# Performance work log

Measured on AMD Instinct MI355X. Metric: run time of the kernel, lower is better.

## Reference

```python
import jax, jax.numpy as jnp
import numpy as np

H = 768
NH = 12
HD = 64
FF = 3072
EPS = 1e-12


def layer_norm(x, g, b):
    mu = jnp.mean(x, axis=-1, keepdims=True)
    var = jnp.mean((x - mu) ** 2, axis=-1, keepdims=True)
    return (x - mu) * jax.lax.rsqrt(var + EPS) * g + b


def setup_inputs() -> dict:
    key = jax.random.key(0)
    ks = jax.random.split(key, 16)
    B, S, L = 16, 512, 50
    s = 0.02
    return {
        "hidden_states": jax.random.normal(ks[0], (B, S, H), jnp.float32),
        "attention_mask": jnp.zeros((B, 1, 1, S), jnp.float32),
        "past_key": jax.random.normal(ks[1], (B, NH, L, HD), jnp.float32),
        "past_value": jax.random.normal(ks[2], (B, NH, L, HD), jnp.float32),
        "Wq": jax.random.normal(ks[3], (H, H), jnp.float32) * s,
        "bq": jnp.zeros((H,), jnp.float32),
        "Wk": jax.random.normal(ks[4], (H, H), jnp.float32) * s,
        "bk": jnp.zeros((H,), jnp.float32),
        "Wv": jax.random.normal(ks[5], (H, H), jnp.float32) * s,
        "bv": jnp.zeros((H,), jnp.float32),
        "Wo": jax.random.normal(ks[6], (H, H), jnp.float32) * s,
        "bo": jnp.zeros((H,), jnp.float32),
        "ln1_g": jnp.ones((H,), jnp.float32),
        "ln1_b": jnp.zeros((H,), jnp.float32),
        "Wi": jax.random.normal(ks[7], (H, FF), jnp.float32) * s,
        "bi": jnp.zeros((FF,), jnp.float32),
        "Wf": jax.random.normal(ks[8], (FF, H), jnp.float32) * s,
        "bf": jnp.zeros((H,), jnp.float32),
        "ln2_g": jnp.ones((H,), jnp.float32),
        "ln2_b": jnp.zeros((H,), jnp.float32),
    }


def reference(hidden_states, attention_mask, past_key, past_value,
              Wq, bq, Wk, bk, Wv, bv, Wo, bo, ln1_g, ln1_b,
              Wi, bi, Wf, bf, ln2_g, ln2_b):
    B, S, _ = hidden_states.shape
    L = past_key.shape[2]

    def heads(x):  # [B,S,H] -> [B,NH,S,HD]
        return x.reshape(B, S, NH, HD).transpose(0, 2, 1, 3)

    q = heads(hidden_states @ Wq + bq)
    k = heads(hidden_states @ Wk + bk)
    v = heads(hidden_states @ Wv + bv)

    # faithful to source bug: past_key_values[0] concatenated into BOTH k and v
    k = jnp.concatenate([past_key, k], axis=2)  # [B,NH,L+S,HD]
    v = jnp.concatenate([past_key, v], axis=2)

    scores = jnp.einsum('bhqd,bhkd->bhqk', q, k) / jnp.sqrt(jnp.float32(HD))
    # visual mask positions get +1.0 (torch.ones), faithful to source
    vis_mask = jnp.ones((B, 1, 1, L), scores.dtype)
    full_mask = jnp.concatenate([vis_mask, attention_mask], axis=-1)
    scores = scores + full_mask

    probs = jax.nn.softmax(scores, axis=-1)
    ctx = jnp.einsum('bhqk,bhkd->bhqd', probs, v)  # [B,NH,S,HD]
    ctx = ctx.transpose(0, 2, 1, 3).reshape(B, S, H)

    attn_out = layer_norm(ctx @ Wo + bo + hidden_states, ln1_g, ln1_b)

    inter = jax.nn.gelu(attn_out @ Wi + bi, approximate=False)
    layer_out = layer_norm(inter @ Wf + bf + attn_out, ln2_g, ln2_b)
    return layer_out
```

## Files before the change

### kernel.cpp

```cpp
#include <hip/hip_runtime.h>
#include <math.h>

#define HDIM 64
#define NHEAD 12
#define HDN 768
#define QKVN 2304
#define FFDIM 3072
#define LPAST 50
#define SEQ 512
#define NBATCH 16
#define TKV (LPAST + SEQ)
#define TKVP 576
#define MTOK (NBATCH * SEQ)
#define NBH (NBATCH * NHEAD)

typedef __attribute__((ext_vector_type(8))) short short8;
typedef __attribute__((ext_vector_type(4))) float f32x4;

__device__ __forceinline__ ushort f2bf(float x) {
    union { float f; unsigned u; } c; c.f = x;
    unsigned r = (c.u + 0x7fffu + ((c.u >> 16) & 1u)) >> 16;
    return (ushort)r;
}
__device__ __forceinline__ float bf2f(ushort u) { return __uint_as_float((unsigned)u << 16); }
__device__ __forceinline__ float geluf(float v) {
    return 0.5f * v * (1.0f + erff(v * 0.70710678118654752f));
}

#define GLOAD_LDS16(gsrc, ldst)                                                    \
    __builtin_amdgcn_global_load_lds(                                              \
        (const __attribute__((address_space(1))) void*)(gsrc),                     \
        (__attribute__((address_space(3))) void*)(ldst), 16, 0, 0)

__global__ __launch_bounds__(256) void prep(
    const float* __restrict__ hs, ushort* __restrict__ hs_bf,
    const float* __restrict__ bq, const float* __restrict__ bk,
    const float* __restrict__ bv, float* __restrict__ bqkv,
    const float* __restrict__ Wq, const float* __restrict__ Wk,
    const float* __restrict__ Wv, const float* __restrict__ Wo,
    ushort* __restrict__ WqT, ushort* __restrict__ WkT,
    ushort* __restrict__ WvT, ushort* __restrict__ WoT,
    const float* __restrict__ Wi, ushort* __restrict__ WiT,
    const float* __restrict__ Wf, ushort* __restrict__ WfT)
{
    __shared__ float tls[32][33];
    int bid = blockIdx.x;
    const int tid = threadIdx.x;

    if (bid < 6144) {
        int i = bid * 256 + tid;
        float4 v = ((const float4*)hs)[i];
        ushort4 o; o.x = f2bf(v.x); o.y = f2bf(v.y); o.z = f2bf(v.z); o.w = f2bf(v.w);
        ((ushort4*)hs_bf)[i] = o;
        return;
    }
    bid -= 6144;
    if (bid < 9) {
        int i = bid * 256 + tid;
        bqkv[i] = i < HDN ? bq[i] : (i < 2 * HDN ? bk[i - HDN] : bv[i - 2 * HDN]);
        return;
    }
    bid -= 9;

    const float* W; ushort* WT; int K, N, bx, by;
    if (bid < 2304) {
        int z = bid / 576, r = bid % 576;
        W = z == 0 ? Wq : z == 1 ? Wk : z == 2 ? Wv : Wo;
        WT = z == 0 ? WqT : z == 1 ? WkT : z == 2 ? WvT : WoT;
        K = HDN; N = HDN; bx = r % 24; by = r / 24;
    } else if (bid < 4608) {
        int r = bid - 2304; W = Wi; WT = WiT; K = HDN; N = FFDIM; bx = r % 96; by = r / 96;
    } else {
        int r = bid - 4608; W = Wf; WT = WfT; K = FFDIM; N = HDN; bx = r % 24; by = r / 24;
    }
    const int n0 = bx * 32, k0 = by * 32;
    const int tx = tid & 31, ty = tid >> 5;
    #pragma unroll
    for (int i = 0; i < 4; ++i)
        tls[ty + i * 8][tx] = W[(size_t)(k0 + ty + i * 8) * N + n0 + tx];
    __syncthreads();
    #pragma unroll
    for (int i = 0; i < 4; ++i)
        WT[(size_t)(n0 + ty + i * 8) * K + k0 + tx] = f2bf(tls[tx][ty + i * 8]);
}

template<int EPI, int BN>
__global__ __launch_bounds__(256, BN == 64 ? 4 : 2) void gemm_t(
    const ushort* __restrict__ A, const ushort* __restrict__ B,
    int lda, int ldb,
    const float* __restrict__ bias, const float* __restrict__ resid,
    const ushort* __restrict__ resid_bf,
    ushort* __restrict__ Cout, int M, int N, int K)
{
    constexpr int NF = BN / 32;
    constexpr int NBG = BN / 64;
    constexpr int BUFU = 4096 + BN * 32;
    __shared__ ushort sm[3 * BUFU];

    const int tid = threadIdx.x;
    const int lane = tid & 63;
    const int wv = tid >> 6;
    const int wr = wv >> 1, wc = wv & 1;
    const int bm = blockIdx.x * 128, bn = blockIdx.y * BN;
    const int lr = lane & 15, lg = lane >> 4;
    const int swzu = ((lr * 64 + lg * 16) ^ ((lr & 8) << 2)) >> 1;
    const size_t kzoff = (size_t)blockIdx.z * K;

    int arow[2], akk[2], brow[NBG], bkk[NBG];
    #pragma unroll
    for (int r = 0; r < 2; ++r) {
        int o = (tid + 256 * r) * 16;
        int st = o >> 10, q = o & 1023;
        q ^= ((q >> 9) & 1) << 5;
        arow[r] = st * 16 + (q >> 6);
        akk[r] = (q & 63) >> 1;
    }
    #pragma unroll
    for (int r = 0; r < NBG; ++r) {
        int o = (tid + 256 * r) * 16;
        int st = o >> 10, q = o & 1023;
        q ^= ((q >> 9) & 1) << 5;
        brow[r] = st * 16 + (q >> 6);
        bkk[r] = (q & 63) >> 1;
    }
    const ushort* Abase = A + (size_t)bm * lda + kzoff;
    const ushort* Bbase = B + (size_t)bn * ldb + kzoff;
    const int nt = K >> 5;

    f32x4 acc[4][NF] = {};

#define STAGE(T, BUF)                                                            \
    do {                                                                         \
        const int k0_ = (T) << 5;                                                \
        char* base_ = (char*)(sm + (BUF) * BUFU);                                \
        _Pragma("unroll")                                                        \
        for (int r_ = 0; r_ < 2; ++r_)                                           \
            GLOAD_LDS16(Abase + (size_t)arow[r_] * lda + k0_ + akk[r_],          \
                        base_ + (tid + 256 * r_) * 16);                          \
        _Pragma("unroll")                                                        \
        for (int r_ = 0; r_ < NBG; ++r_)                                         \
            GLOAD_LDS16(Bbase + (size_t)brow[r_] * ldb + k0_ + bkk[r_],          \
                        base_ + 8192 + (tid + 256 * r_) * 16);                   \
    } while (0)

    STAGE(0, 0);
    STAGE(1, 1);
    if (BN == 128) asm volatile("s_waitcnt vmcnt(4)" ::: "memory");
    else           asm volatile("s_waitcnt vmcnt(3)" ::: "memory");
    __builtin_amdgcn_sched_barrier(0);
    __builtin_amdgcn_s_barrier();
    __builtin_amdgcn_sched_barrier(0);

    int buf = 0;
    for (int t = 0; t < nt; ++t) {
        if (t + 2 < nt) {
            int nbuf = buf + 2; if (nbuf >= 3) nbuf -= 3;
            STAGE(t + 2, nbuf);
        }
        const ushort* ab = sm + buf * BUFU;
        short8 af[4], bfv[NF];
        #pragma unroll
        for (int i = 0; i < 4; ++i)
            af[i] = *(const short8*)(ab + (wr * 4 + i) * 512 + swzu);
        #pragma unroll
        for (int j = 0; j < NF; ++j)
            bfv[j] = *(const short8*)(ab + 4096 + (wc * NF + j) * 512 + swzu);
        __builtin_amdgcn_s_setprio(1);
        #pragma unroll
        for (int i = 0; i < 4; ++i)
            #pragma unroll
            for (int j = 0; j < NF; ++j)
                acc[i][j] = __builtin_amdgcn_mfma_f32_16x16x32_bf16(
                    af[i], bfv[j], acc[i][j], 0, 0, 0);
        __builtin_amdgcn_s_setprio(0);
        if (t + 2 < nt) {
            if (BN == 128) asm volatile("s_waitcnt vmcnt(4)" ::: "memory");
            else           asm volatile("s_waitcnt vmcnt(3)" ::: "memory");
        } else {
            asm volatile("s_waitcnt vmcnt(0)" ::: "memory");
        }
        __builtin_amdgcn_sched_barrier(0);
        __builtin_amdgcn_s_barrier();
        __builtin_amdgcn_sched_barrier(0);
        buf = buf + 1 == 3 ? 0 : buf + 1;
    }
#undef STAGE

    ushort* Cz = Cout + (size_t)blockIdx.z * M * N;
    #pragma unroll
    for (int i = 0; i < 4; ++i) {
        #pragma unroll
        for (int j = 0; j < NF; ++j) {
            const int col = bn + wc * (BN / 2) + j * 16 + lr;
            float bv = 0.0f;
            if (EPI != 5) bv = bias[col];
            #pragma unroll
            for (int rr = 0; rr < 4; ++rr) {
                const int row = bm + wr * 64 + i * 16 + lg * 4 + rr;
                const size_t idx = (size_t)row * N + col;
                float v = acc[i][j][rr] + bv;
                if (EPI == 1) v += resid[idx];
                if (EPI == 4) v += bf2f(resid_bf[idx]);
                if (EPI == 2) v = geluf(v);
                Cz[idx] = f2bf(v);
            }
        }
    }
}

__global__ __launch_bounds__(256) void kvAll(
    const ushort* __restrict__ qkv, const float* __restrict__ past_key,
    ushort* __restrict__ kf, ushort* __restrict__ vt)
{
    __shared__ ushort td[64][72];
    const int bh = blockIdx.x / 9;
    const int t0 = (blockIdx.x % 9) * 64;
    const int b = bh / NHEAD, h = bh % NHEAD;
    const int trow = threadIdx.x >> 2, seg = threadIdx.x & 3;
    const int t = t0 + trow;

    ushort kv16[16], vv16[16];
    if (t < LPAST) {
        const float* pk = past_key + ((size_t)bh * LPAST + t) * HDIM + seg * 16;
        #pragma unroll
        for (int i = 0; i < 4; ++i) {
            float4 f = ((const float4*)pk)[i];
            kv16[i * 4 + 0] = f2bf(f.x); kv16[i * 4 + 1] = f2bf(f.y);
            kv16[i * 4 + 2] = f2bf(f.z); kv16[i * 4 + 3] = f2bf(f.w);
        }
        #pragma unroll
        for (int i = 0; i < 16; ++i) vv16[i] = kv16[i];
    } else if (t < TKV) {
        const ushort* kp = qkv + ((size_t)(b * SEQ + (t - LPAST))) * QKVN
                               + HDN + h * HDIM + seg * 16;
        *(uint4*)&kv16[0] = ((const uint4*)kp)[0];
        *(uint4*)&kv16[8] = ((const uint4*)kp)[1];
        const ushort* vp = kp + HDN;
        *(uint4*)&vv16[0] = ((const uint4*)vp)[0];
        *(uint4*)&vv16[8] = ((const uint4*)vp)[1];
    } else {
        #pragma unroll
        for (int i = 0; i < 16; ++i) { kv16[i] = 0; vv16[i] = 0; }
    }

    if (t < TKV) {
        ushort* kd = kf + (((size_t)bh * TKV + t) << 6) + seg * 16;
        *(uint4*)kd = *(uint4*)&kv16[0];
        *(uint4*)(kd + 8) = *(uint4*)&kv16[8];
    }

    #pragma unroll
    for (int i = 0; i < 16; ++i) td[trow][seg * 16 + i] = vv16[i];
    __syncthreads();

    const int d = threadIdx.x >> 2;
    ushort o[16];
    #pragma unroll
    for (int i = 0; i < 16; ++i) o[i] = td[seg * 16 + i][d];
    ushort* dst = vt + ((size_t)bh * HDIM + d) * TKVP + t0 + seg * 16;
    *(uint4*)dst = *(uint4*)&o[0];
    *(uint4*)(dst + 8) = *(uint4*)&o[8];
}

__global__ __launch_bounds__(256) void attn4(
    const ushort* __restrict__ qkv, const ushort* __restrict__ kf,
    const ushort* __restrict__ vt, const float* __restrict__ mask,
    ushort* __restrict__ ctx)
{
    __shared__ ushort Ks[64 * 64];
    __shared__ ushort Vs[64 * 64];
    __shared__ ushort Ps[4][16 * 64];

    const int wv = threadIdx.x >> 6, lane = threadIdx.x & 63;
    const int lr = lane & 15, lg = lane >> 4;
    const int bid = blockIdx.x;
    const int xcd = bid & 7, gi = bid >> 3;
    const int bh = xcd * (NBH / 8) + (gi >> 3);
    const int s0 = (gi & 7) * 64;
    const int b = bh / NHEAD, h = bh % NHEAD;

    short8 af[2];
    {
        const ushort* qp = qkv + ((size_t)(b * SEQ + s0 + wv * 16 + lr)) * QKVN
                               + h * HDIM + lg * 8;
        af[0] = *(const short8*)qp;
        af[1] = *(const short8*)(qp + 32);
    }

    const ushort* kbase = kf + (size_t)bh * TKV * HDIM;
    const ushort* vbase = vt + (size_t)bh * HDIM * TKVP;

    float l[4] = {};
    f32x4 ctxa[4] = {};

    for (int kt = 0; kt < 9; ++kt) {
        const int t0 = kt * 64;
        #pragma unroll
        for (int r = 0; r < 2; ++r) {
            int sl = (int)threadIdx.x + 256 * r;
            int row = sl >> 3, p = sl & 7;
            int j = p ^ (row & 7);
            int trow = t0 + row; if (trow > TKV - 1) trow = TKV - 1;
            GLOAD_LDS16(kbase + ((size_t)trow << 6) + j * 8, (char*)Ks + sl * 16);
        }
        #pragma unroll
        for (int r = 0; r < 2; ++r) {
            int sl = (int)threadIdx.x + 256 * r;
            int row = sl >> 3, p = sl & 7;
            int j = p ^ (row & 7);
            GLOAD_LDS16(vbase + (size_t)row * TKVP + t0 + j * 8, (char*)Vs + sl * 16);
        }
        __syncthreads();

        f32x4 sa[4] = {};
        #pragma unroll
        for (int kb = 0; kb < 4; ++kb) {
            const int key = kb * 16 + lr;
            #pragma unroll
            for (int c = 0; c < 2; ++c) {
                const int phys = (c * 4 + lg) ^ (key & 7);
                short8 kfrag = *(const short8*)&Ks[key * 64 + phys * 8];
                sa[kb] = __builtin_amdgcn_mfma_f32_16x16x32_bf16(
                    af[c], kfrag, sa[kb], 0, 0, 0);
            }
        }

        #pragma unroll
        for (int kb = 0; kb < 4; ++kb) {
            const int t = t0 + kb * 16 + lr;
            float addv;
            if (t >= TKV) addv = -1e30f;
            else addv = ((t < LPAST) ? 1.0f : mask[(size_t)b * SEQ + (t - LPAST)]) - 4.0f;
            const int key = kb * 16 + lr;
            #pragma unroll
            for (int r = 0; r < 4; ++r) {
                float p = __expf(fmaf(sa[kb][r], 0.125f, addv));
                l[r] += p;
                const int q_ = lg * 4 + r;
                const int phys = (key >> 3) ^ (q_ & 7);
                Ps[wv][q_ * 64 + phys * 8 + (key & 7)] = f2bf(p);
            }
        }

        short8 pa[2];
        #pragma unroll
        for (int c = 0; c < 2; ++c) {
            const int phys = (c * 4 + lg) ^ (lr & 7);
            pa[c] = *(const short8*)&Ps[wv][lr * 64 + phys * 8];
        }
        #pragma unroll
        for (int dg = 0; dg < 4; ++dg) {
            const int d = dg * 16 + lr;
            #pragma unroll
            for (int c = 0; c < 2; ++c) {
                const int phys = (c * 4 + lg) ^ (d & 7);
                short8 vfrag = *(const short8*)&Vs[d * 64 + phys * 8];
                ctxa[dg] = __builtin_amdgcn_mfma_f32_16x16x32_bf16(
                    pa[c], vfrag, ctxa[dg], 0, 0, 0);
            }
        }
        __syncthreads();
    }

    #pragma unroll
    for (int r = 0; r < 4; ++r) {
        float s = l[r];
        s += __shfl_xor(s, 1); s += __shfl_xor(s, 2);
        s += __shfl_xor(s, 4); s += __shfl_xor(s, 8);
        l[r] = 1.0f / s;
    }
    #pragma unroll
    for (int r = 0; r < 4; ++r) {
        const int q_ = s0 + wv * 16 + lg * 4 + r;
        const size_t base = ((size_t)(b * SEQ + q_)) * HDN + h * HDIM;
        #pragma unroll
        for (int dg = 0; dg < 4; ++dg)
            ctx[base + dg * 16 + lr] = f2bf(ctxa[dg][r] * l[r]);
    }
}

__global__ __launch_bounds__(256) void layernorm3(
    const ushort* __restrict__ x, const float* __restrict__ g,
    const float* __restrict__ b, float* __restrict__ out,
    ushort* __restrict__ out_bf)
{
    const size_t row = blockIdx.x;
    const ushort* xr = &x[row * HDN];
    const int t = threadIdx.x;

    float v0 = bf2f(xr[t]), v1 = bf2f(xr[t + 256]), v2 = bf2f(xr[t + 512]);

    __shared__ float red[4];
    float s = v0 + v1 + v2;
    #pragma unroll
    for (int off = 32; off > 0; off >>= 1) s += __shfl_xor(s, off);
    if ((t & 63) == 0) red[t >> 6] = s;
    __syncthreads();
    float mean = (red[0] + red[1] + red[2] + red[3]) * (1.0f / 768.0f);

    float d0 = v0 - mean, d1 = v1 - mean, d2 = v2 - mean;
    float vs = d0 * d0 + d1 * d1 + d2 * d2;
    #pragma unroll
    for (int off = 32; off > 0; off >>= 1) vs += __shfl_xor(vs, off);
    __syncthreads();
    if ((t & 63) == 0) red[t >> 6] = vs;
    __syncthreads();
    float var = (red[0] + red[1] + red[2] + red[3]) * (1.0f / 768.0f);
    float rstd = rsqrtf(var + 1e-12f);

    float o0 = d0 * rstd * g[t] + b[t];
    float o1 = d1 * rstd * g[t + 256] + b[t + 256];
    float o2 = d2 * rstd * g[t + 512] + b[t + 512];
    if (out) {
        out[row * HDN + t] = o0;
        out[row * HDN + t + 256] = o1;
        out[row * HDN + t + 512] = o2;
    }
    if (out_bf) {
        out_bf[row * HDN + t] = f2bf(o0);
        out_bf[row * HDN + t + 256] = f2bf(o1);
        out_bf[row * HDN + t + 512] = f2bf(o2);
    }
}

__global__ __launch_bounds__(256) void ln_red(
    const ushort* __restrict__ p0, const ushort* __restrict__ p1,
    const float* __restrict__ bias, const ushort* __restrict__ resid,
    const float* __restrict__ g, const float* __restrict__ b,
    float* __restrict__ out)
{
    const size_t row = blockIdx.x;
    const size_t base = row * HDN;
    const int t = threadIdx.x;

    float v0 = bf2f(p0[base + t])       + bf2f(p1[base + t])       + bias[t]       + bf2f(resid[base + t]);
    float v1 = bf2f(p0[base + t + 256]) + bf2f(p1[base + t + 256]) + bias[t + 256] + bf2f(resid[base + t + 256]);
    float v2 = bf2f(p0[base + t + 512]) + bf2f(p1[base + t + 512]) + bias[t + 512] + bf2f(resid[base + t + 512]);

    __shared__ float red[4];
    float s = v0 + v1 + v2;
    #pragma unroll
    for (int off = 32; off > 0; off >>= 1) s += __shfl_xor(s, off);
    if ((t & 63) == 0) red[t >> 6] = s;
    __syncthreads();
    float mean = (red[0] + red[1] + red[2] + red[3]) * (1.0f / 768.0f);

    float d0 = v0 - mean, d1 = v1 - mean, d2 = v2 - mean;
    float vs = d0 * d0 + d1 * d1 + d2 * d2;
    #pragma unroll
    for (int off = 32; off > 0; off >>= 1) vs += __shfl_xor(vs, off);
    __syncthreads();
    if ((t & 63) == 0) red[t >> 6] = vs;
    __syncthreads();
    float var = (red[0] + red[1] + red[2] + red[3]) * (1.0f / 768.0f);
    float rstd = rsqrtf(var + 1e-12f);

    out[base + t]       = d0 * rstd * g[t]       + b[t];
    out[base + t + 256] = d1 * rstd * g[t + 256] + b[t + 256];
    out[base + t + 512] = d2 * rstd * g[t + 512] + b[t + 512];
}

extern "C" void kernel_launch(void* const* d_in, const int* in_sizes, int n_in,
                              void* d_out, int out_size, void* d_ws, size_t ws_size,
                              hipStream_t stream) {
    const float* hs       = (const float*)d_in[0];
    const float* mask     = (const float*)d_in[1];
    const float* past_key = (const float*)d_in[2];
    const float* Wq = (const float*)d_in[4];
    const float* bq = (const float*)d_in[5];
    const float* Wk = (const float*)d_in[6];
    const float* bk = (const float*)d_in[7];
    const float* Wv = (const float*)d_in[8];
    const float* bv = (const float*)d_in[9];
    const float* Wo = (const float*)d_in[10];
    const float* bo = (const float*)d_in[11];
    const float* ln1_g = (const float*)d_in[12];
    const float* ln1_b = (const float*)d_in[13];
    const float* Wi = (const float*)d_in[14];
    const float* bi = (const float*)d_in[15];
    const float* Wf = (const float*)d_in[16];
    const float* bf_ = (const float*)d_in[17];
    const float* ln2_g = (const float*)d_in[18];
    const float* ln2_b = (const float*)d_in[19];
    float* out = (float*)d_out;

    char* w = (char*)d_ws;
    ushort* WqT   = (ushort*)(w + 0);
    ushort* WoT   = (ushort*)(w + 3538944);
    ushort* WiT   = (ushort*)(w + 4718592);
    ushort* WfT   = (ushort*)(w + 9437184);
    float*  bqkv  = (float*)(w + 14155776);
    ushort* hs_bf = (ushort*)(w + 14172160);
    ushort* qkv   = (ushort*)(w + 26755072);
    ushort* kf    = (ushort*)(w + 64503808);
    ushort* vt    = (ushort*)(w + 78315520);
    ushort* ctx_bf = hs_bf;
    ushort* tmp_bf = (ushort*)(w + 64503808);
    ushort* inter  = (ushort*)(w + 14172160);
    ushort* pbuf   = (ushort*)(w + 64503808);
    ushort* aln_bf = (ushort*)(w + 89669632);
    ushort* WkT = WqT + (size_t)HDN * HDN;
    ushort* WvT = WqT + (size_t)2 * HDN * HDN;

    dim3 b256(256);

    prep<<<dim3(13065), b256, 0, stream>>>(
        hs, hs_bf, bq, bk, bv, bqkv,
        Wq, Wk, Wv, Wo, WqT, WkT, WvT, WoT, Wi, WiT, Wf, WfT);

    gemm_t<0, 128><<<dim3(MTOK / 128, QKVN / 128), b256, 0, stream>>>(
        hs_bf, WqT, HDN, HDN, bqkv, nullptr, nullptr, qkv, MTOK, QKVN, HDN);

    kvAll<<<dim3(NBH * 9), b256, 0, stream>>>(qkv, past_key, kf, vt);

    attn4<<<dim3(NBH * 8), b256, 0, stream>>>(qkv, kf, vt, mask, ctx_bf);

    gemm_t<1, 64><<<dim3(MTOK / 128, HDN / 64), b256, 0, stream>>>(
        ctx_bf, WoT, HDN, HDN, bo, hs, nullptr, tmp_bf, MTOK, HDN, HDN);
    layernorm3<<<dim3(MTOK), b256, 0, stream>>>(tmp_bf, ln1_g, ln1_b, nullptr, aln_bf);

    gemm_t<2, 128><<<dim3(MTOK / 128, FFDIM / 128), b256, 0, stream>>>(
        aln_bf, WiT, HDN, HDN, bi, nullptr, nullptr, inter, MTOK, FFDIM, HDN);
    gemm_t<5, 128><<<dim3(MTOK / 128, HDN / 128, 2), b256, 0, stream>>>(
        inter, WfT, FFDIM, FFDIM, nullptr, nullptr, nullptr, pbuf, MTOK, HDN, FFDIM / 2);

    ln_red<<<dim3(MTOK), b256, 0, stream>>>(
        pbuf, pbuf + (size_t)MTOK * HDN, bf_, aln_bf, ln2_g, ln2_b, out);
}
```

Before: 245.9 us.

## Double-buffer K/V tiles and process two query tiles per attention block

The attention kernel now prefetches the next K/V tile into a second LDS buffer while computing on the current one. It also handles 128 queries per block instead of 64, so each loaded K/V tile is reused twice and global K/V traffic is halved. The cost is double the LDS for K/V, more registers for two accumulator sets, and half as many blocks, which reduces parallelism across the GPU.

After: 247.8 us. Within noise of the previous version (+0.8%).

```diff
diff --git a/kernel.cpp b/kernel.cpp
--- a/kernel.cpp
+++ b/kernel.cpp
@@ -262,120 +262,155 @@
     *(uint4*)(dst + 8) = *(uint4*)&o[8];
 }
 
-__global__ __launch_bounds__(256) void attn4(
+__global__ __launch_bounds__(256) void attn5(
     const ushort* __restrict__ qkv, const ushort* __restrict__ kf,
     const ushort* __restrict__ vt, const float* __restrict__ mask,
     ushort* __restrict__ ctx)
 {
-    __shared__ ushort Ks[64 * 64];
-    __shared__ ushort Vs[64 * 64];
+    __shared__ ushort Ks[2][64 * 64];
+    __shared__ ushort Vs[2][64 * 64];
     __shared__ ushort Ps[4][16 * 64];
 
     const int wv = threadIdx.x >> 6, lane = threadIdx.x & 63;
     const int lr = lane & 15, lg = lane >> 4;
     const int bid = blockIdx.x;
     const int xcd = bid & 7, gi = bid >> 3;
-    const int bh = xcd * (NBH / 8) + (gi >> 3);
-    const int s0 = (gi & 7) * 64;
+    const int bh = xcd * (NBH / 8) + (gi >> 2);
+    const int s0 = (gi & 3) * 128;
     const int b = bh / NHEAD, h = bh % NHEAD;
 
-    short8 af[2];
+    short8 af0[2], af1[2];
     {
         const ushort* qp = qkv + ((size_t)(b * SEQ + s0 + wv * 16 + lr)) * QKVN
                                + h * HDIM + lg * 8;
-        af[0] = *(const short8*)qp;
-        af[1] = *(const short8*)(qp + 32);
+        af0[0] = *(const short8*)qp;
+        af0[1] = *(const short8*)(qp + 32);
+        const ushort* qp1 = qp + (size_t)64 * QKVN;
+        af1[0] = *(const short8*)qp1;
+        af1[1] = *(const short8*)(qp1 + 32);
     }
 
     const ushort* kbase = kf + (size_t)bh * TKV * HDIM;
     const ushort* vbase = vt + (size_t)bh * HDIM * TKVP;
 
-    float l[4] = {};
-    f32x4 ctxa[4] = {};
+    float l0[4] = {}, l1[4] = {};
+    f32x4 c0[4] = {}, c1[4] = {};
+
+#define ASTAGE(KT, BUF)                                                         \
+    do {                                                                        \
+        const int t0_ = (KT) * 64;                                              \
+        _Pragma("unroll")                                                       \
+        for (int r = 0; r < 2; ++r) {                                           \
+            int sl = (int)threadIdx.x + 256 * r;                                \
+            int row = sl >> 3, p = sl & 7;                                      \
+            int j = p ^ (row & 7);                                              \
+            int trow = t0_ + row; if (trow > TKV - 1) trow = TKV - 1;           \
+            GLOAD_LDS16(kbase + ((size_t)trow << 6) + j * 8,                    \
+                        (char*)Ks[BUF] + sl * 16);                              \
+        }                                                                       \
+        _Pragma("unroll")                                                       \
+        for (int r = 0; r < 2; ++r) {                                           \
+            int sl = (int)threadIdx.x + 256 * r;                                \
+            int row = sl >> 3, p = sl & 7;                                      \
+            int j = p ^ (row & 7);                                              \
+            GLOAD_LDS16(vbase + (size_t)row * TKVP + t0_ + j * 8,               \
+                        (char*)Vs[BUF] + sl * 16);                              \
+        }                                                                       \
+    } while (0)
+
+#define QKPV(AF, L, C)                                                          \
+    do {                                                                        \
+        f32x4 sa[4] = {};                                                       \
+        _Pragma("unroll")                                                       \
+        for (int kb = 0; kb < 4; ++kb) {                                        \
+            const int key = kb * 16 + lr;                                       \
+            _Pragma("unroll")                                                   \
+            for (int c = 0; c < 2; ++c) {                                       \
+                const int phys = (c * 4 + lg) ^ (key & 7);                      \
+                short8 kfrag = *(const short8*)&Ks[buf][key * 64 + phys * 8];   \
+                sa[kb] = __builtin_amdgcn_mfma_f32_16x16x32_bf16(               \
+                    AF[c], kfrag, sa[kb], 0, 0, 0);                             \
+            }                                                                   \
+        }                                                                       \
+        _Pragma("unroll")                                                       \
+        for (int kb = 0; kb < 4; ++kb) {                                        \
+            const int t = t0 + kb * 16 + lr;                                    \
+            float addv;                                                         \
+            if (t >= TKV) addv = -1e30f;                                        \
+            else addv = ((t < LPAST) ? 1.0f                                     \
+                         : mask[(size_t)b * SEQ + (t - LPAST)]) - 4.0f;         \
+            const int key = kb * 16 + lr;                                       \
+            _Pragma("unroll")                                                   \
+            for (int r = 0; r < 4; ++r) {                                       \
+                float p = __expf(fmaf(sa[kb][r], 0.125f, addv));                \
+                L[r] += p;                                                      \
+                const int q_ = lg * 4 + r;                                      \
+                const int phys = (key >> 3) ^ (q_ & 7);                         \
+                Ps[wv][q_ * 64 + phys * 8 + (key & 7)] = f2bf(p);               \
+            }                                                                   \
+        }                                                                       \
+        short8 pa[2];                                                           \
+        _Pragma("unroll")                                                       \
+        for (int c = 0; c < 2; ++c) {                                           \
+            const int phys = (c * 4 + lg) ^ (lr & 7);                           \
+            pa[c] = *(const short8*)&Ps[wv][lr * 64 + phys * 8];                \
+        }                                                                       \
+        _Pragma("unroll")                                                       \
+        for (int dg = 0; dg < 4; ++dg) {                                        \
+            const int d = dg * 16 + lr;                                         \
+            _Pragma("unroll")                                                   \
+            for (int c = 0; c < 2; ++c) {                                       \
+                const int phys = (c * 4 + lg) ^ (d & 7);                        \
+                short8 vfrag = *(const short8*)&Vs[buf][d * 64 + phys * 8];     \
+                C[dg] = __builtin_amdgcn_mfma_f32_16x16x32_bf16(                \
+                    pa[c], vfrag, C[dg], 0, 0, 0);                              \
+            }                                                                   \
+        }                                                                       \
+    } while (0)
+
+    ASTAGE(0, 0);
+    asm volatile("s_waitcnt vmcnt(0)" ::: "memory");
+    __builtin_amdgcn_sched_barrier(0);
+    __builtin_amdgcn_s_barrier();
+    __builtin_amdgcn_sched_barrier(0);
 
     for (int kt = 0; kt < 9; ++kt) {
+        const int buf = kt & 1;
         const int t0 = kt * 64;
-        #pragma unroll
-        for (int r = 0; r < 2; ++r) {
-            int sl = (int)threadIdx.x + 256 * r;
-            int row = sl >> 3, p = sl & 7;
-            int j = p ^ (row & 7);
-            int trow = t0 + row; if (trow > TKV - 1) trow = TKV - 1;
-            GLOAD_LDS16(kbase + ((size_t)trow << 6) + j * 8, (char*)Ks + sl * 16);
-        }
-        #pragma unroll
-        for (int r = 0; r < 2; ++r) {
-            int sl = (int)threadIdx.x + 256 * r;
-            int row = sl >> 3, p = sl & 7;
-            int j = p ^ (row & 7);
-            GLOAD_LDS16(vbase + (size_t)row * TKVP + t0 + j * 8, (char*)Vs + sl * 16);
-        }
-        __syncthreads();
-
-        f32x4 sa[4] = {};
-        #pragma unroll
-        for (int kb = 0; kb < 4; ++kb) {
-            const int key = kb * 16 + lr;
-            #pragma unroll
-            for (int c = 0; c < 2; ++c) {
-                const int phys = (c * 4 + lg) ^ (key & 7);
-                short8 kfrag = *(const short8*)&Ks[key * 64 + phys * 8];
-                sa[kb] = __builtin_amdgcn_mfma_f32_16x16x32_bf16(
-                    af[c], kfrag, sa[kb], 0, 0, 0);
-            }
-        }
-
-        #pragma unroll
-        for (int kb = 0; kb < 4; ++kb) {
-            const int t = t0 + kb * 16 + lr;
-            float addv;
-            if (t >= TKV) addv = -1e30f;
-            else addv = ((t < LPAST) ? 1.0f : mask[(size_t)b * SEQ + (t - LPAST)]) - 4.0f;
-            const int key = kb * 16 + lr;
-            #pragma unroll
-            for (int r = 0; r < 4; ++r) {
-                float p = __expf(fmaf(sa[kb][r], 0.125f, addv));
-                l[r] += p;
-                const int q_ = lg * 4 + r;
-                const int phys = (key >> 3) ^ (q_ & 7);
-                Ps[wv][q_ * 64 + phys * 8 + (key & 7)] = f2bf(p);
-            }
-        }
-
-        short8 pa[2];
-        #pragma unroll
-        for (int c = 0; c < 2; ++c) {
-            const int phys = (c * 4 + lg) ^ (lr & 7);
-            pa[c] = *(const short8*)&Ps[wv][lr * 64 + phys * 8];
-        }
-        #pragma unroll
-        for (int dg = 0; dg < 4; ++dg) {
-            const int d = dg * 16 + lr;
-            #pragma unroll
-            for (int c = 0; c < 2; ++c) {
-                const int phys = (c * 4 + lg) ^ (d & 7);
-                short8 vfrag = *(const short8*)&Vs[d * 64 + phys * 8];
-                ctxa[dg] = __builtin_amdgcn_mfma_f32_16x16x32_bf16(
-                    pa[c], vfrag, ctxa[dg], 0, 0, 0);
-            }
-        }
-        __syncthreads();
-    }
+        if (kt < 8) ASTAGE(kt + 1, buf ^ 1);
+
+        QKPV(af0, l0, c0);
+        QKPV(af1, l1, c1);
+
+        asm volatile("s_waitcnt vmcnt(0)" ::: "memory");
+        __builtin_amdgcn_sched_barrier(0);
+        __builtin_amdgcn_s_barrier();
+        __builtin_amdgcn_sched_barrier(0);
+    }
+#undef QKPV
+#undef ASTAGE
 
     #pragma unroll
     for (int r = 0; r < 4; ++r) {
-        float s = l[r];
+        float s = l0[r];
         s += __shfl_xor(s, 1); s += __shfl_xor(s, 2);
         s += __shfl_xor(s, 4); s += __shfl_xor(s, 8);
-        l[r] = 1.0f / s;
+        l0[r] = 1.0f / s;
+        float s1 = l1[r];
+        s1 += __shfl_xor(s1, 1); s1 += __shfl_xor(s1, 2);
+        s1 += __shfl_xor(s1, 4); s1 += __shfl_xor(s1, 8);
+        l1[r] = 1.0f / s1;
     }
     #pragma unroll
     for (int r = 0; r < 4; ++r) {
         const int q_ = s0 + wv * 16 + lg * 4 + r;
-        const size_t base = ((size_t)(b * SEQ + q_)) * HDN + h * HDIM;
-        #pragma unroll
-        for (int dg = 0; dg < 4; ++dg)
-            ctx[base + dg * 16 + lr] = f2bf(ctxa[dg][r] * l[r]);
+        const size_t base0 = ((size_t)(b * SEQ + q_)) * HDN + h * HDIM;
+        const size_t base1 = ((size_t)(b * SEQ + q_ + 64)) * HDN + h * HDIM;
+        #pragma unroll
+        for (int dg = 0; dg < 4; ++dg) {
+            ctx[base0 + dg * 16 + lr] = f2bf(c0[dg][r] * l0[r]);
+            ctx[base1 + dg * 16 + lr] = f2bf(c1[dg][r] * l1[r]);
+        }
     }
 }
 
@@ -513,7 +548,7 @@
 
     kvAll<<<dim3(NBH * 9), b256, 0, stream>>>(qkv, past_key, kf, vt);
 
-    attn4<<<dim3(NBH * 8), b256, 0, stream>>>(qkv, kf, vt, mask, ctx_bf);
+    attn5<<<dim3(NBH * 4), b256, 0, stream>>>(qkv, kf, vt, mask, ctx_bf);
 
     gemm_t<1, 64><<<dim3(MTOK / 128, HDN / 64), b256, 0, stream>>>(
         ctx_bf, WoT, HDN, HDN, bo, hs, nullptr, tmp_bf, MTOK, HDN, HDN);
```

## Double the GEMM K-tile to 64 with double buffering instead of triple

Applied to the files above, without the earlier changes.

The bf16 MFMA GEMM now stages 64-wide K slices, as two 32-wide halves, into two LDS buffers instead of 32-wide slices into three buffers. This halves the number of loop iterations and block barriers and gives each wave twice as many MFMAs per barrier. In exchange, prefetch depth drops from two stages ahead to one, each iteration waits on vmcnt(0), and per-block LDS and register use rise. Occupancy for the BN=64 variant is lowered from 4 to 3 to fit.

After: 246.4 us. Within noise of the previous version (+0.2%).

```diff
diff --git a/kernel.cpp b/kernel.cpp
--- a/kernel.cpp
+++ b/kernel.cpp
@@ -85,7 +85,7 @@
 }
 
 template<int EPI, int BN>
-__global__ __launch_bounds__(256, BN == 64 ? 4 : 2) void gemm_t(
+__global__ __launch_bounds__(256, BN == 64 ? 3 : 2) void gemm_t(
     const ushort* __restrict__ A, const ushort* __restrict__ B,
     int lda, int ldb,
     const float* __restrict__ bias, const float* __restrict__ resid,
@@ -93,9 +93,11 @@
     ushort* __restrict__ Cout, int M, int N, int K)
 {
     constexpr int NF = BN / 32;
-    constexpr int NBG = BN / 64;
-    constexpr int BUFU = 4096 + BN * 32;
-    __shared__ ushort sm[3 * BUFU];
+    constexpr int NBL = BN / 32;
+    constexpr int BHS = BN * 4;
+    constexpr int BHU = BN * 32;
+    constexpr int BUFU = 8192 + BN * 64;
+    __shared__ ushort sm[2 * BUFU];
 
     const int tid = threadIdx.x;
     const int lane = tid & 63;
@@ -106,83 +108,84 @@
     const int swzu = ((lr * 64 + lg * 16) ^ ((lr & 8) << 2)) >> 1;
     const size_t kzoff = (size_t)blockIdx.z * K;
 
-    int arow[2], akk[2], brow[NBG], bkk[NBG];
-    #pragma unroll
-    for (int r = 0; r < 2; ++r) {
-        int o = (tid + 256 * r) * 16;
+    int arow[4], akk[4], brow[NBL], bkk[NBL];
+    #pragma unroll
+    for (int r = 0; r < 4; ++r) {
+        int sl = tid + 256 * r;
+        int half = sl >> 9, within = sl & 511;
+        int o = within * 16;
         int st = o >> 10, q = o & 1023;
         q ^= ((q >> 9) & 1) << 5;
         arow[r] = st * 16 + (q >> 6);
-        akk[r] = (q & 63) >> 1;
-    }
-    #pragma unroll
-    for (int r = 0; r < NBG; ++r) {
-        int o = (tid + 256 * r) * 16;
+        akk[r] = half * 32 + ((q & 63) >> 1);
+    }
+    #pragma unroll
+    for (int r = 0; r < NBL; ++r) {
+        int sl = tid + 256 * r;
+        int half = sl / BHS, within = sl % BHS;
+        int o = within * 16;
         int st = o >> 10, q = o & 1023;
         q ^= ((q >> 9) & 1) << 5;
         brow[r] = st * 16 + (q >> 6);
-        bkk[r] = (q & 63) >> 1;
+        bkk[r] = half * 32 + ((q & 63) >> 1);
     }
     const ushort* Abase = A + (size_t)bm * lda + kzoff;
     const ushort* Bbase = B + (size_t)bn * ldb + kzoff;
-    const int nt = K >> 5;
+    const int nt = K >> 6;
 
     f32x4 acc[4][NF] = {};
 
 #define STAGE(T, BUF)                                                            \
     do {                                                                         \
-        const int k0_ = (T) << 5;                                                \
+        const int k0_ = (T) << 6;                                                \
         char* base_ = (char*)(sm + (BUF) * BUFU);                                \
         _Pragma("unroll")                                                        \
-        for (int r_ = 0; r_ < 2; ++r_)                                           \
+        for (int r_ = 0; r_ < 4; ++r_)                                           \
             GLOAD_LDS16(Abase + (size_t)arow[r_] * lda + k0_ + akk[r_],          \
                         base_ + (tid + 256 * r_) * 16);                          \
         _Pragma("unroll")                                                        \
-        for (int r_ = 0; r_ < NBG; ++r_)                                         \
+        for (int r_ = 0; r_ < NBL; ++r_)                                         \
             GLOAD_LDS16(Bbase + (size_t)brow[r_] * ldb + k0_ + bkk[r_],          \
-                        base_ + 8192 + (tid + 256 * r_) * 16);                   \
+                        base_ + 16384 + (tid + 256 * r_) * 16);                  \
     } while (0)
 
     STAGE(0, 0);
-    STAGE(1, 1);
-    if (BN == 128) asm volatile("s_waitcnt vmcnt(4)" ::: "memory");
-    else           asm volatile("s_waitcnt vmcnt(3)" ::: "memory");
+    asm volatile("s_waitcnt vmcnt(0)" ::: "memory");
     __builtin_amdgcn_sched_barrier(0);
     __builtin_amdgcn_s_barrier();
     __builtin_amdgcn_sched_barrier(0);
 
     int buf = 0;
     for (int t = 0; t < nt; ++t) {
-        if (t + 2 < nt) {
-            int nbuf = buf + 2; if (nbuf >= 3) nbuf -= 3;
-            STAGE(t + 2, nbuf);
-        }
+        if (t + 1 < nt) STAGE(t + 1, buf ^ 1);
         const ushort* ab = sm + buf * BUFU;
-        short8 af[4], bfv[NF];
+        short8 af[4][2], bfv[NF][2];
         #pragma unroll
         for (int i = 0; i < 4; ++i)
-            af[i] = *(const short8*)(ab + (wr * 4 + i) * 512 + swzu);
+            #pragma unroll
+            for (int h = 0; h < 2; ++h)
+                af[i][h] = *(const short8*)(ab + h * 4096 + (wr * 4 + i) * 512 + swzu);
         #pragma unroll
         for (int j = 0; j < NF; ++j)
-            bfv[j] = *(const short8*)(ab + 4096 + (wc * NF + j) * 512 + swzu);
+            #pragma unroll
+            for (int h = 0; h < 2; ++h)
+                bfv[j][h] = *(const short8*)(ab + 8192 + h * BHU + (wc * NF + j) * 512 + swzu);
         __builtin_amdgcn_s_setprio(1);
         #pragma unroll
         for (int i = 0; i < 4; ++i)
             #pragma unroll
-            for (int j = 0; j < NF; ++j)
+            for (int j = 0; j < NF; ++j) {
                 acc[i][j] = __builtin_amdgcn_mfma_f32_16x16x32_bf16(
-                    af[i], bfv[j], acc[i][j], 0, 0, 0);
+                    af[i][0], bfv[j][0], acc[i][j], 0, 0, 0);
+                acc[i][j] = __builtin_amdgcn_mfma_f32_16x16x32_bf16(
+                    af[i][1], bfv[j][1], acc[i][j], 0, 0, 0);
+            }
         __builtin_amdgcn_s_setprio(0);
-        if (t + 2 < nt) {
-            if (BN == 128) asm volatile("s_waitcnt vmcnt(4)" ::: "memory");
-            else           asm volatile("s_waitcnt vmcnt(3)" ::: "memory");
-        } else {
-            asm volatile("s_waitcnt vmcnt(0)" ::: "memory");
-        }
+        asm volatile("s_waitcnt vmcnt(0)" ::: "memory");
         __builtin_amdgcn_sched_barrier(0);
         __builtin_amdgcn_s_barrier();
         __builtin_amdgcn_sched_barrier(0);
-        buf = buf + 1 == 3 ? 0 : buf + 1;
+        buf ^= 1;
     }
 #undef STAGE
 
```
